# Kernel optimization log

Measured on AMD Instinct MI355X. Metric: run time of the kernel, lower is better.

Reference implementation:

```python
import jax, jax.numpy as jnp
import numpy as np

N, NQ, NV, NE = 4, 256, 512, 256


def setup_inputs() -> dict:
    key = jax.random.key(0)
    ks = jax.random.split(key, 6)
    scale = 1.0 / np.sqrt(NE)
    return {
        "query": jax.random.normal(ks[0], (N, NQ, NE), dtype=jnp.float32),
        "context": jax.random.normal(ks[1], (N, NV, NE), dtype=jnp.float32),
        "memory": jax.random.normal(ks[2], (N, NV, NE), dtype=jnp.float32),
        "w_logit": jax.random.normal(ks[3], (NE,), dtype=jnp.float32) * scale,
        "b_logit": jnp.zeros((), dtype=jnp.float32),
        "temp": jnp.ones((), dtype=jnp.float32),
        "w_reduce": jax.random.normal(ks[4], (NE, NE), dtype=jnp.float32) * scale,
        "b_reduce": jnp.zeros((NE,), dtype=jnp.float32),
    }


def reference(query, context, memory, w_logit, b_logit, temp, w_reduce, b_reduce):
    # Additive (Bahdanau) attention, single-head branch of the torch module.
    # qc: [N, nQ, nV, nE] -- the large broadcast-add + tanh intermediate
    qc = jnp.tanh(query[:, :, None, :] + context[:, None, :, :])
    # fc_logit: Linear(nE -> 1), squeeze last dim -> [N, nQ, nV]
    logits = jnp.einsum("nqve,e->nqv", qc, w_logit) + b_logit
    probs = jax.nn.softmax(logits / temp, axis=2)
    # bmm(probs, memory) -> [N, nQ, nE], then leaky_relu (torch default slope 0.01)
    heads = jax.nn.leaky_relu(jnp.einsum("nqv,nve->nqe", probs, memory), negative_slope=0.01)
    # fc_reduceheads: Linear(nE -> nE), torch semantics y = x @ W.T + b
    return heads @ w_reduce.T + b_reduce
```

## Files before the change

### kernel.cpp

```cpp
#include <hip/hip_runtime.h>
#include <math.h>

#define N_B   4
#define NQ_   256
#define NV_   512
#define NE_   256

#define QSCALE 2.8853900817779268f
#define QTF 4

__device__ __forceinline__ float wave_reduce_sum(float v) {
#pragma unroll
    for (int m = 32; m > 0; m >>= 1) v += __shfl_xor(v, m, 64);
    return v;
}

__global__ __launch_bounds__(256) void prep_kernel(const float* __restrict__ C,
                                                   const float* __restrict__ W,
                                                   float* __restrict__ EC,
                                                   float* __restrict__ WT) {
    __shared__ float tile[64][65];
    const int b = blockIdx.x;
    const int col = threadIdx.x & 63, row4 = threadIdx.x >> 6;
    if (b < 128) {
        const int n  = b >> 5;
        const int e0 = ((b >> 3) & 3) * 64;
        const int v0 = (b & 7) * 64;
        const float* src = C + ((size_t)n * NV_ + v0) * NE_ + e0;
#pragma unroll
        for (int r = 0; r < 16; ++r) {
            const int vl = row4 + r * 4;
            tile[vl][col] = __builtin_amdgcn_exp2f(src[(size_t)vl * NE_ + col] * QSCALE);
        }
        __syncthreads();
        float2* dst = (float2*)EC + ((size_t)n * (NE_ / 2) + (e0 >> 1)) * NV_ + v0;
#pragma unroll
        for (int rr = 0; rr < 8; ++rr) {
            const int pe = rr * 4 + row4;
            dst[(size_t)pe * NV_ + col] =
                make_float2(tile[col][2 * pe], tile[col][2 * pe + 1]);
        }
    } else {
        const int bb = b - 128;
        const int r0 = (bb >> 2) * 64, c0 = (bb & 3) * 64;
        const float* src = W + (size_t)r0 * NE_ + c0;
#pragma unroll
        for (int r = 0; r < 16; ++r) {
            const int rl = row4 + r * 4;
            tile[rl][col] = src[(size_t)rl * NE_ + col];
        }
        __syncthreads();
        float* dst = WT + (size_t)c0 * NE_ + r0;
#pragma unroll
        for (int r = 0; r < 16; ++r) {
            const int cl = row4 + r * 4;
            dst[(size_t)cl * NE_ + col] = tile[col][cl];
        }
    }
}

#define FMA4(h, p, m)                  \
    h.x = fmaf(p, m.x, h.x);           \
    h.y = fmaf(p, m.y, h.y);           \
    h.z = fmaf(p, m.z, h.z);           \
    h.w = fmaf(p, m.w, h.w)

__global__ __launch_bounds__(1024) void fused_attn(
    const float* __restrict__ Q,
    const float* __restrict__ EC,
    const float* __restrict__ WL,
    const float* __restrict__ M,
    const float* __restrict__ TEMP,
    const float* __restrict__ WRT,
    const float* __restrict__ BR,
    float* __restrict__ OUT)
{
    const int n   = blockIdx.y;
    const int q0  = blockIdx.x * QTF;
    const int tid = threadIdx.x;
    const int wv  = tid >> 6, ln = tid & 63;

    __shared__ __align__(16) float s_q[NE_][QTF];
    __shared__ __align__(16) float s_w[NE_];
    __shared__ __align__(16) float s_prob[QTF][NV_];
    __shared__ __align__(16) float s_sp[QTF][NV_];
    __shared__ __align__(16) float s_part[16][QTF][NE_];
    __shared__ __align__(16) float s_heads[QTF][NE_];
    __shared__ __align__(16) float s_gp[QTF][NE_];
    __shared__ float s_sum[QTF][8];

    {
        const int e = tid & 255;
        const int g = tid >> 8;
        s_q[e][g] = __builtin_amdgcn_exp2f(
            Q[((size_t)n * NQ_ + q0 + g) * NE_ + e] * QSCALE);
        if (g == 0) s_w[e] = WL[e];
    }
    __syncthreads();

    const int v  = tid & 511;
    const int eh = tid >> 9;
    float acc0 = 0.f, acc1 = 0.f, acc2 = 0.f, acc3 = 0.f;
    {
        const float2* ec2 =
            (const float2*)EC + ((size_t)n * (NE_ / 2) + eh * 64) * NV_ + v;
#pragma unroll 4
        for (int pe = 0; pe < 64; ++pe) {
            const float2 c = ec2[(size_t)pe * NV_];
            const int e = eh * 128 + 2 * pe;
            const float4 qa = *(const float4*)s_q[e];
            const float4 qb = *(const float4*)s_q[e + 1];
            const float2 w  = *(const float2*)&s_w[e];
            {
                const float a = fmaf(c.x, qa.x, 1.0f);
                const float b = fmaf(c.y, qb.x, 1.0f);
                const float num = fmaf(w.y, a, w.x * b);
                acc0 = fmaf(num, __builtin_amdgcn_rcpf(a * b), acc0);
            }
            {
                const float a = fmaf(c.x, qa.y, 1.0f);
                const float b = fmaf(c.y, qb.y, 1.0f);
                const float num = fmaf(w.y, a, w.x * b);
                acc1 = fmaf(num, __builtin_amdgcn_rcpf(a * b), acc1);
            }
            {
                const float a = fmaf(c.x, qa.z, 1.0f);
                const float b = fmaf(c.y, qb.z, 1.0f);
                const float num = fmaf(w.y, a, w.x * b);
                acc2 = fmaf(num, __builtin_amdgcn_rcpf(a * b), acc2);
            }
            {
                const float a = fmaf(c.x, qa.w, 1.0f);
                const float b = fmaf(c.y, qb.w, 1.0f);
                const float num = fmaf(w.y, a, w.x * b);
                acc3 = fmaf(num, __builtin_amdgcn_rcpf(a * b), acc3);
            }
        }
    }
    if (eh) {
        s_sp[0][v] = acc0; s_sp[1][v] = acc1;
        s_sp[2][v] = acc2; s_sp[3][v] = acc3;
    }
    __syncthreads();

    float p0 = 0.f, p1 = 0.f, p2 = 0.f, p3 = 0.f;
    if (!eh) {
        const float scale = -2.0f / TEMP[0];
        p0 = __expf((acc0 + s_sp[0][v]) * scale);
        p1 = __expf((acc1 + s_sp[1][v]) * scale);
        p2 = __expf((acc2 + s_sp[2][v]) * scale);
        p3 = __expf((acc3 + s_sp[3][v]) * scale);
        const float r0 = wave_reduce_sum(p0);
        const float r1 = wave_reduce_sum(p1);
        const float r2 = wave_reduce_sum(p2);
        const float r3 = wave_reduce_sum(p3);
        if (ln == 0) {
            s_sum[0][wv] = r0; s_sum[1][wv] = r1;
            s_sum[2][wv] = r2; s_sum[3][wv] = r3;
        }
    }
    __syncthreads();
    if (!eh) {
        float t0 = 0.f, t1 = 0.f, t2 = 0.f, t3 = 0.f;
#pragma unroll
        for (int w = 0; w < 8; ++w) {
            t0 += s_sum[0][w]; t1 += s_sum[1][w];
            t2 += s_sum[2][w]; t3 += s_sum[3][w];
        }
        s_prob[0][v] = p0 * (1.0f / t0);
        s_prob[1][v] = p1 * (1.0f / t1);
        s_prob[2][v] = p2 * (1.0f / t2);
        s_prob[3][v] = p3 * (1.0f / t3);
    }
    __syncthreads();

    {
        const float4* M4 = (const float4*)(M + (size_t)n * NV_ * NE_);
        float4 h0 = make_float4(0.f, 0.f, 0.f, 0.f);
        float4 h1 = h0, h2 = h0, h3 = h0;
        const int v0w = wv * 32;
#pragma unroll 2
        for (int vb = v0w; vb < v0w + 32; vb += 4) {
            const float4 pq0 = *(const float4*)&s_prob[0][vb];
            const float4 pq1 = *(const float4*)&s_prob[1][vb];
            const float4 pq2 = *(const float4*)&s_prob[2][vb];
            const float4 pq3 = *(const float4*)&s_prob[3][vb];
            float4 mm;
            mm = M4[(size_t)(vb + 0) * (NE_ / 4) + ln];
            FMA4(h0, pq0.x, mm); FMA4(h1, pq1.x, mm);
            FMA4(h2, pq2.x, mm); FMA4(h3, pq3.x, mm);
            mm = M4[(size_t)(vb + 1) * (NE_ / 4) + ln];
            FMA4(h0, pq0.y, mm); FMA4(h1, pq1.y, mm);
            FMA4(h2, pq2.y, mm); FMA4(h3, pq3.y, mm);
            mm = M4[(size_t)(vb + 2) * (NE_ / 4) + ln];
            FMA4(h0, pq0.z, mm); FMA4(h1, pq1.z, mm);
            FMA4(h2, pq2.z, mm); FMA4(h3, pq3.z, mm);
            mm = M4[(size_t)(vb + 3) * (NE_ / 4) + ln];
            FMA4(h0, pq0.w, mm); FMA4(h1, pq1.w, mm);
            FMA4(h2, pq2.w, mm); FMA4(h3, pq3.w, mm);
        }
        ((float4*)s_part[wv][0])[ln] = h0;
        ((float4*)s_part[wv][1])[ln] = h1;
        ((float4*)s_part[wv][2])[ln] = h2;
        ((float4*)s_part[wv][3])[ln] = h3;
    }
    __syncthreads();

    {
        const int t = tid >> 8, e = tid & 255;
        float s = 0.f;
#pragma unroll
        for (int w = 0; w < 16; ++w) s += s_part[w][t][e];
        s_heads[t][e] = (s > 0.0f) ? s : 0.01f * s;
    }
    __syncthreads();

    {
        const int eh2 = tid >> 9;
        const int tg  = ((tid >> 8) & 1) * 2;
        const int ep  = tid & 255;
        const float* wc = WRT + ep;
        float a0 = 0.f, a1 = 0.f;
        const int e0g = eh2 * 128;
#pragma unroll 8
        for (int e = e0g; e < e0g + 128; ++e) {
            const float ww = wc[(size_t)e * NE_];
            a0 = fmaf(s_heads[tg][e], ww, a0);
            a1 = fmaf(s_heads[tg + 1][e], ww, a1);
        }
        if (eh2) { s_gp[tg][ep] = a0; s_gp[tg + 1][ep] = a1; }
        __syncthreads();
        if (!eh2) {
            const float b = BR[ep];
            OUT[((size_t)n * NQ_ + q0 + tg) * NE_ + ep]     = a0 + s_gp[tg][ep] + b;
            OUT[((size_t)n * NQ_ + q0 + tg + 1) * NE_ + ep] = a1 + s_gp[tg + 1][ep] + b;
        }
    }
}

extern "C" void kernel_launch(void* const* d_in, const int* in_sizes, int n_in,
                              void* d_out, int out_size, void* d_ws, size_t ws_size,
                              hipStream_t stream) {
    const float* Q  = (const float*)d_in[0];
    const float* C  = (const float*)d_in[1];
    const float* M  = (const float*)d_in[2];
    const float* WL = (const float*)d_in[3];
    const float* T  = (const float*)d_in[5];
    const float* WR = (const float*)d_in[6];
    const float* BR = (const float*)d_in[7];
    float* OUT = (float*)d_out;

    float* EC  = (float*)d_ws;
    float* WRT = EC + (size_t)N_B * NE_ * NV_;

    prep_kernel<<<dim3(144), 256, 0, stream>>>(C, WR, EC, WRT);

    dim3 gf(NQ_ / QTF, N_B);
    fused_attn<<<gf, 1024, 0, stream>>>(Q, EC, WL, M, T, WRT, BR, OUT);
}
```

Baseline: 99.62 us.

## Vectorize context loads, rebalance pair/single reciprocals, defer softmax normalization

Context exponentials are now stored in groups of four along the embedding axis, so the logit loop reads one float4 per step. Each group of four quads pairs three quads into shared reciprocals and handles the fourth with one reciprocal per element, to rebalance transcendental and VALU work. Softmax normalization moves into the heads reduction, which removes one block barrier, and the exponent uses exp2 directly. The final reduce GEMV is reorganized so each thread accumulates a float4 of outputs over a quarter of the embedding axis, and the partials are combined in shared memory.

```diff
diff --git a/kernel.cpp b/kernel.cpp
--- a/kernel.cpp
+++ b/kernel.cpp
@@ -21,28 +21,36 @@
                                                    float* __restrict__ WT) {
     __shared__ float tile[64][65];
     const int b = blockIdx.x;
-    const int col = threadIdx.x & 63, row4 = threadIdx.x >> 6;
     if (b < 128) {
         const int n  = b >> 5;
         const int e0 = ((b >> 3) & 3) * 64;
         const int v0 = (b & 7) * 64;
         const float* src = C + ((size_t)n * NV_ + v0) * NE_ + e0;
-#pragma unroll
-        for (int r = 0; r < 16; ++r) {
-            const int vl = row4 + r * 4;
-            tile[vl][col] = __builtin_amdgcn_exp2f(src[(size_t)vl * NE_ + col] * QSCALE);
+        const int c4 = (threadIdx.x & 15) * 4;
+        const int r  = threadIdx.x >> 4;
+#pragma unroll
+        for (int it = 0; it < 4; ++it) {
+            const int vl = it * 16 + r;
+            const float4 x = *(const float4*)(src + (size_t)vl * NE_ + c4);
+            tile[vl][c4 + 0] = __builtin_amdgcn_exp2f(x.x * QSCALE);
+            tile[vl][c4 + 1] = __builtin_amdgcn_exp2f(x.y * QSCALE);
+            tile[vl][c4 + 2] = __builtin_amdgcn_exp2f(x.z * QSCALE);
+            tile[vl][c4 + 3] = __builtin_amdgcn_exp2f(x.w * QSCALE);
         }
         __syncthreads();
-        float2* dst = (float2*)EC + ((size_t)n * (NE_ / 2) + (e0 >> 1)) * NV_ + v0;
-#pragma unroll
-        for (int rr = 0; rr < 8; ++rr) {
-            const int pe = rr * 4 + row4;
-            dst[(size_t)pe * NV_ + col] =
-                make_float2(tile[col][2 * pe], tile[col][2 * pe + 1]);
+        const int vcol = threadIdx.x & 63, row4 = threadIdx.x >> 6;
+        float4* dst = (float4*)EC + ((size_t)n * (NE_ / 4) + (e0 >> 2)) * NV_ + v0;
+#pragma unroll
+        for (int rr = 0; rr < 4; ++rr) {
+            const int qd = rr * 4 + row4;
+            dst[(size_t)qd * NV_ + vcol] =
+                make_float4(tile[vcol][4 * qd + 0], tile[vcol][4 * qd + 1],
+                            tile[vcol][4 * qd + 2], tile[vcol][4 * qd + 3]);
         }
     } else {
         const int bb = b - 128;
         const int r0 = (bb >> 2) * 64, c0 = (bb & 3) * 64;
+        const int col = threadIdx.x & 63, row4 = threadIdx.x >> 6;
         const float* src = W + (size_t)r0 * NE_ + c0;
 #pragma unroll
         for (int r = 0; r < 16; ++r) {
@@ -64,6 +72,37 @@
     h.y = fmaf(p, m.y, h.y);           \
     h.z = fmaf(p, m.z, h.z);           \
     h.w = fmaf(p, m.w, h.w)
+
+#define PAIR(c0, c1, ebase) {                                        \
+    const float4 qa = *(const float4*)s_q[(ebase)];                  \
+    const float4 qb = *(const float4*)s_q[(ebase) + 1];              \
+    const float w0 = s_w[(ebase)], w1 = s_w[(ebase) + 1];            \
+    { const float a = fmaf((c0), qa.x, 1.0f);                        \
+      const float b = fmaf((c1), qb.x, 1.0f);                        \
+      const float num = fmaf(w1, a, w0 * b);                         \
+      acc0 = fmaf(num, __builtin_amdgcn_rcpf(a * b), acc0); }        \
+    { const float a = fmaf((c0), qa.y, 1.0f);                        \
+      const float b = fmaf((c1), qb.y, 1.0f);                        \
+      const float num = fmaf(w1, a, w0 * b);                         \
+      acc1 = fmaf(num, __builtin_amdgcn_rcpf(a * b), acc1); }        \
+    { const float a = fmaf((c0), qa.z, 1.0f);                        \
+      const float b = fmaf((c1), qb.z, 1.0f);                        \
+      const float num = fmaf(w1, a, w0 * b);                         \
+      acc2 = fmaf(num, __builtin_amdgcn_rcpf(a * b), acc2); }        \
+    { const float a = fmaf((c0), qa.w, 1.0f);                        \
+      const float b = fmaf((c1), qb.w, 1.0f);                        \
+      const float num = fmaf(w1, a, w0 * b);                         \
+      acc3 = fmaf(num, __builtin_amdgcn_rcpf(a * b), acc3); }        \
+}
+
+#define UNP(c, ebase) {                                              \
+    const float4 qa = *(const float4*)s_q[(ebase)];                  \
+    const float w = s_w[(ebase)];                                    \
+    acc0 = fmaf(w, __builtin_amdgcn_rcpf(fmaf((c), qa.x, 1.0f)), acc0); \
+    acc1 = fmaf(w, __builtin_amdgcn_rcpf(fmaf((c), qa.y, 1.0f)), acc1); \
+    acc2 = fmaf(w, __builtin_amdgcn_rcpf(fmaf((c), qa.z, 1.0f)), acc2); \
+    acc3 = fmaf(w, __builtin_amdgcn_rcpf(fmaf((c), qa.w, 1.0f)), acc3); \
+}
 
 __global__ __launch_bounds__(1024) void fused_attn(
     const float* __restrict__ Q,
@@ -86,7 +125,7 @@
     __shared__ __align__(16) float s_sp[QTF][NV_];
     __shared__ __align__(16) float s_part[16][QTF][NE_];
     __shared__ __align__(16) float s_heads[QTF][NE_];
-    __shared__ __align__(16) float s_gp[QTF][NE_];
+    __shared__ __align__(16) float4 s_gp4[3][QTF][64];
     __shared__ float s_sum[QTF][8];
 
     {
@@ -102,38 +141,25 @@
     const int eh = tid >> 9;
     float acc0 = 0.f, acc1 = 0.f, acc2 = 0.f, acc3 = 0.f;
     {
-        const float2* ec2 =
-            (const float2*)EC + ((size_t)n * (NE_ / 2) + eh * 64) * NV_ + v;
-#pragma unroll 4
-        for (int pe = 0; pe < 64; ++pe) {
-            const float2 c = ec2[(size_t)pe * NV_];
-            const int e = eh * 128 + 2 * pe;
-            const float4 qa = *(const float4*)s_q[e];
-            const float4 qb = *(const float4*)s_q[e + 1];
-            const float2 w  = *(const float2*)&s_w[e];
-            {
-                const float a = fmaf(c.x, qa.x, 1.0f);
-                const float b = fmaf(c.y, qb.x, 1.0f);
-                const float num = fmaf(w.y, a, w.x * b);
-                acc0 = fmaf(num, __builtin_amdgcn_rcpf(a * b), acc0);
+        const float4* ecq =
+            (const float4*)EC + ((size_t)n * (NE_ / 4) + eh * 32) * NV_ + v;
+#pragma unroll 2
+        for (int g = 0; g < 8; ++g) {
+            const int qb = g * 4;
+#pragma unroll
+            for (int j = 0; j < 3; ++j) {
+                const float4 c4 = ecq[(size_t)(qb + j) * NV_];
+                const int e = eh * 128 + (qb + j) * 4;
+                PAIR(c4.x, c4.y, e);
+                PAIR(c4.z, c4.w, e + 2);
             }
             {
-                const float a = fmaf(c.x, qa.y, 1.0f);
-                const float b = fmaf(c.y, qb.y, 1.0f);
-                const float num = fmaf(w.y, a, w.x * b);
-                acc1 = fmaf(num, __builtin_amdgcn_rcpf(a * b), acc1);
-            }
-            {
-                const float a = fmaf(c.x, qa.z, 1.0f);
-                const float b = fmaf(c.y, qb.z, 1.0f);
-                const float num = fmaf(w.y, a, w.x * b);
-                acc2 = fmaf(num, __builtin_amdgcn_rcpf(a * b), acc2);
-            }
-            {
-                const float a = fmaf(c.x, qa.w, 1.0f);
-                const float b = fmaf(c.y, qb.w, 1.0f);
-                const float num = fmaf(w.y, a, w.x * b);
-                acc3 = fmaf(num, __builtin_amdgcn_rcpf(a * b), acc3);
+                const float4 c4 = ecq[(size_t)(qb + 3) * NV_];
+                const int e = eh * 128 + (qb + 3) * 4;
+                UNP(c4.x, e);
+                UNP(c4.y, e + 1);
+                UNP(c4.z, e + 2);
+                UNP(c4.w, e + 3);
             }
         }
     }
@@ -143,13 +169,14 @@
     }
     __syncthreads();
 
-    float p0 = 0.f, p1 = 0.f, p2 = 0.f, p3 = 0.f;
     if (!eh) {
-        const float scale = -2.0f / TEMP[0];
-        p0 = __expf((acc0 + s_sp[0][v]) * scale);
-        p1 = __expf((acc1 + s_sp[1][v]) * scale);
-        p2 = __expf((acc2 + s_sp[2][v]) * scale);
-        p3 = __expf((acc3 + s_sp[3][v]) * scale);
+        const float sE = -2.8853900817779268f / TEMP[0];
+        const float p0 = __builtin_amdgcn_exp2f((acc0 + s_sp[0][v]) * sE);
+        const float p1 = __builtin_amdgcn_exp2f((acc1 + s_sp[1][v]) * sE);
+        const float p2 = __builtin_amdgcn_exp2f((acc2 + s_sp[2][v]) * sE);
+        const float p3 = __builtin_amdgcn_exp2f((acc3 + s_sp[3][v]) * sE);
+        s_prob[0][v] = p0; s_prob[1][v] = p1;
+        s_prob[2][v] = p2; s_prob[3][v] = p3;
         const float r0 = wave_reduce_sum(p0);
         const float r1 = wave_reduce_sum(p1);
         const float r2 = wave_reduce_sum(p2);
@@ -158,19 +185,6 @@
             s_sum[0][wv] = r0; s_sum[1][wv] = r1;
             s_sum[2][wv] = r2; s_sum[3][wv] = r3;
         }
-    }
-    __syncthreads();
-    if (!eh) {
-        float t0 = 0.f, t1 = 0.f, t2 = 0.f, t3 = 0.f;
-#pragma unroll
-        for (int w = 0; w < 8; ++w) {
-            t0 += s_sum[0][w]; t1 += s_sum[1][w];
-            t2 += s_sum[2][w]; t3 += s_sum[3][w];
-        }
-        s_prob[0][v] = p0 * (1.0f / t0);
-        s_prob[1][v] = p1 * (1.0f / t1);
-        s_prob[2][v] = p2 * (1.0f / t2);
-        s_prob[3][v] = p3 * (1.0f / t3);
     }
     __syncthreads();
 
@@ -211,29 +225,38 @@
         float s = 0.f;
 #pragma unroll
         for (int w = 0; w < 16; ++w) s += s_part[w][t][e];
-        s_heads[t][e] = (s > 0.0f) ? s : 0.01f * s;
-    }
-    __syncthreads();
-
-    {
-        const int eh2 = tid >> 9;
-        const int tg  = ((tid >> 8) & 1) * 2;
-        const int ep  = tid & 255;
-        const float* wc = WRT + ep;
-        float a0 = 0.f, a1 = 0.f;
-        const int e0g = eh2 * 128;
+        float tot = 0.f;
+#pragma unroll
+        for (int w = 0; w < 8; ++w) tot += s_sum[t][w];
+        const float hv = s * (1.0f / tot);
+        s_heads[t][e] = (hv > 0.0f) ? hv : 0.01f * hv;
+    }
+    __syncthreads();
+
+    {
+        const int q   = tid >> 8;
+        const int k   = (tid >> 6) & 3;
+        const int epq = tid & 63;
+        const float4* wr4 = (const float4*)WRT + epq;
+        float4 a = make_float4(0.f, 0.f, 0.f, 0.f);
+        const int e0g = k * 64;
 #pragma unroll 8
-        for (int e = e0g; e < e0g + 128; ++e) {
-            const float ww = wc[(size_t)e * NE_];
-            a0 = fmaf(s_heads[tg][e], ww, a0);
-            a1 = fmaf(s_heads[tg + 1][e], ww, a1);
-        }
-        if (eh2) { s_gp[tg][ep] = a0; s_gp[tg + 1][ep] = a1; }
+        for (int e = e0g; e < e0g + 64; ++e) {
+            const float h = s_heads[q][e];
+            const float4 w4 = wr4[(size_t)e * (NE_ / 4)];
+            FMA4(a, h, w4);
+        }
+        if (k) s_gp4[k - 1][q][epq] = a;
         __syncthreads();
-        if (!eh2) {
-            const float b = BR[ep];
-            OUT[((size_t)n * NQ_ + q0 + tg) * NE_ + ep]     = a0 + s_gp[tg][ep] + b;
-            OUT[((size_t)n * NQ_ + q0 + tg + 1) * NE_ + ep] = a1 + s_gp[tg + 1][ep] + b;
+        if (k == 0) {
+#pragma unroll
+            for (int kk = 0; kk < 3; ++kk) {
+                const float4 p = s_gp4[kk][q][epq];
+                a.x += p.x; a.y += p.y; a.z += p.z; a.w += p.w;
+            }
+            const float4 b4 = ((const float4*)BR)[epq];
+            a.x += b4.x; a.y += b4.y; a.z += b4.z; a.w += b4.w;
+            ((float4*)OUT)[((size_t)n * NQ_ + q0 + q) * (NE_ / 4) + epq] = a;
         }
     }
 }
```

Measured after the change: 103.7 us. 1.04x slower.
